# Kernel optimization log

Measured on AMD Instinct MI355X. Metric: run time of the kernel, lower is better.

## Reference

```python
import jax, jax.numpy as jnp
import numpy as np

B, T, C = 2, 2048, 2048
H, D = 16, 128


def _rope(x, cos, sin):
    # x: [B,H,T,D], cos/sin: [T,D//2]
    half = x.shape[-1] // 2
    x1, x2 = x[..., :half], x[..., half:]
    c = cos[None, None, :, :]
    s = sin[None, None, :, :]
    return jnp.concatenate([x1 * c - x2 * s, x1 * s + x2 * c], axis=-1)


def setup_inputs() -> dict:
    key = jax.random.key(0)
    k1, k2, k3, k4, k5 = jax.random.split(key, 5)
    x = jax.random.normal(k1, (B, T, C), dtype=jnp.float32)
    cos = jax.random.uniform(k2, (T, D // 2), dtype=jnp.float32)
    sin = jax.random.uniform(k3, (T, D // 2), dtype=jnp.float32)
    scale = 1.0 / np.sqrt(C)
    W_qkv = jax.random.normal(k4, (C, 3 * C), dtype=jnp.float32) * scale
    W_proj = jax.random.normal(k5, (C, C), dtype=jnp.float32) * scale
    return {"x": x, "cos": cos, "sin": sin, "W_qkv": W_qkv, "W_proj": W_proj}


def reference(x, cos, sin, W_qkv, W_proj):
    Bx, Tx, Cx = x.shape
    qkv = x @ W_qkv  # [B,T,3C]
    q, k, v = jnp.split(qkv, 3, axis=-1)
    # [B,T,C] -> [B,H,T,D]
    q = q.reshape(Bx, Tx, H, D).transpose(0, 2, 1, 3)
    k = k.reshape(Bx, Tx, H, D).transpose(0, 2, 1, 3)
    v = v.reshape(Bx, Tx, H, D).transpose(0, 2, 1, 3)
    q = _rope(q, cos, sin)
    k = _rope(k, cos, sin)
    # causal SDPA
    scores = jnp.einsum("bhqd,bhkd->bhqk", q, k) / jnp.sqrt(jnp.float32(D))
    causal = jnp.tril(jnp.ones((Tx, Tx), dtype=bool))
    scores = jnp.where(causal[None, None], scores, jnp.finfo(scores.dtype).min)
    attn = jax.nn.softmax(scores, axis=-1)
    out = jnp.einsum("bhqk,bhkd->bhqd", attn, v)
    out = out.transpose(0, 2, 1, 3).reshape(Bx, Tx, Cx)
    return out @ W_proj
```

## Files before the change

kernel.cpp:

```cpp
#include <hip/hip_runtime.h>
#include <stdint.h>

#define B_  2
#define T_  2048
#define C_  2048
#define H_  16
#define D_  128
#define BH_ 32
#define M_  4096

typedef __attribute__((ext_vector_type(8))) __bf16  bf16x8;
typedef __attribute__((ext_vector_type(4))) float   floatx4;
typedef __attribute__((ext_vector_type(4))) ushort  ushortx4;

__device__ __forceinline__ ushort f2bf(float f) {
    union { float f; uint32_t u; } v; v.f = f;
    return (ushort)((v.u + 0x7fffu + ((v.u >> 16) & 1u)) >> 16);
}

__device__ __forceinline__ float bf2f(ushort u) {
    union { uint32_t u; float f; } v; v.u = ((uint32_t)u) << 16;
    return v.f;
}

__device__ __forceinline__ floatx4 mfma_bf16(bf16x8 a, bf16x8 b, floatx4 c) {
    return __builtin_amdgcn_mfma_f32_16x16x32_bf16(a, b, c, 0, 0, 0);
}

__device__ __forceinline__ void async16(const ushort* g, ushort* l) {
    __builtin_amdgcn_global_load_lds(
        (const __attribute__((address_space(1))) uint32_t*)g,
        (__attribute__((address_space(3))) uint32_t*)l, 16, 0, 0);
}

__global__ __launch_bounds__(256) void convert_bf16(
    const float* __restrict__ X, ushort* __restrict__ Xb)
{
    const int i = blockIdx.x * 256 + threadIdx.x;
    const float4 v = ((const float4*)X)[i];
    ushortx4 p = { f2bf(v.x), f2bf(v.y), f2bf(v.z), f2bf(v.w) };
    ((ushortx4*)Xb)[i] = p;
}

__global__ __launch_bounds__(256) void transpose_w(
    const float* __restrict__ W, ushort* __restrict__ Wt, int Kdim, int Ndim)
{
    __shared__ float tile[32][33];
    const int n0 = blockIdx.x * 32, k0 = blockIdx.y * 32;
    const int tx = threadIdx.x, ty = threadIdx.y;
    #pragma unroll
    for (int j = 0; j < 4; j++)
        tile[ty + j*8][tx] = W[(size_t)(k0 + ty + j*8) * Ndim + n0 + tx];
    __syncthreads();
    #pragma unroll
    for (int j = 0; j < 4; j++)
        Wt[(size_t)(n0 + ty + j*8) * Kdim + k0 + tx] = f2bf(tile[tx][ty + j*8]);
}

#define BM 128
#define BN 128
#define BK 32

__global__ __launch_bounds__(256) void gemm_bt(
    const ushort* __restrict__ A, const ushort* __restrict__ Bt,
    float* __restrict__ Co, int Ndim, int Kdim)
{
    __shared__ __align__(16) ushort As[BM * BK];
    __shared__ __align__(16) ushort Bs[BN * BK];
    const int tid  = threadIdx.x;
    const int lane = tid & 63;
    const int w    = tid >> 6;
    const int wm   = (w >> 1) * 64;
    const int wn   = (w & 1) * 64;
    const int lr   = lane & 15;
    const int quad = lane >> 4;
    const int srow = lane >> 2;
    const int soff = (lane & 3) * 8;

    const ushort* Ablk = A  + (size_t)(blockIdx.y * BM) * Kdim;
    const ushort* Bblk = Bt + (size_t)(blockIdx.x * BN) * Kdim;

    floatx4 acc[4][4];
    #pragma unroll
    for (int i = 0; i < 4; i++)
        #pragma unroll
        for (int j = 0; j < 4; j++)
            acc[i][j] = (floatx4){0.f, 0.f, 0.f, 0.f};

    for (int k0 = 0; k0 < Kdim; k0 += BK) {
        __syncthreads();
        #pragma unroll
        for (int j = 0; j < 2; j++) {
            const int row = w * 32 + j * 16 + srow;
            async16(Ablk + (size_t)row * Kdim + k0 + soff,
                    As + (w * 32 + j * 16) * BK);
            async16(Bblk + (size_t)row * Kdim + k0 + soff,
                    Bs + (w * 32 + j * 16) * BK);
        }
        __syncthreads();

        bf16x8 af[4], bfr[4];
        #pragma unroll
        for (int mi = 0; mi < 4; mi++)
            af[mi] = *(const bf16x8*)(&As[(wm + mi*16 + lr) * BK + quad * 8]);
        #pragma unroll
        for (int ni = 0; ni < 4; ni++)
            bfr[ni] = *(const bf16x8*)(&Bs[(wn + ni*16 + lr) * BK + quad * 8]);
        #pragma unroll
        for (int mi = 0; mi < 4; mi++)
            #pragma unroll
            for (int ni = 0; ni < 4; ni++)
                acc[mi][ni] = mfma_bf16(af[mi], bfr[ni], acc[mi][ni]);
    }

    const size_t row0 = (size_t)blockIdx.y * BM + wm;
    const size_t col0 = (size_t)blockIdx.x * BN + wn;
    #pragma unroll
    for (int mi = 0; mi < 4; mi++)
        #pragma unroll
        for (int ni = 0; ni < 4; ni++)
            #pragma unroll
            for (int r = 0; r < 4; r++)
                Co[(row0 + mi*16 + quad*4 + r) * (size_t)Ndim + col0 + ni*16 + lr]
                    = acc[mi][ni][r];
}

__global__ __launch_bounds__(256) void gemm_qkv(
    const ushort* __restrict__ A, const ushort* __restrict__ Bt,
    const float* __restrict__ cosb, const float* __restrict__ sinb,
    ushort* __restrict__ qb, ushort* __restrict__ kbf, ushort* __restrict__ vt)
{
    __shared__ __align__(16) ushort smem[17408];
    ushort* As = smem;
    ushort* Bs = smem + 4096;

    const int tid  = threadIdx.x;
    const int lane = tid & 63;
    const int w    = tid >> 6;
    const int wm   = (w >> 1) * 64;
    const int wn   = (w & 1) * 64;
    const int lr   = lane & 15;
    const int quad = lane >> 4;
    const int srow = lane >> 2;
    const int soff = (lane & 3) * 8;

    const int Kdim = C_;
    const ushort* Ablk = A  + (size_t)(blockIdx.y * BM) * Kdim;
    const ushort* Bblk = Bt + (size_t)(blockIdx.x * BN) * Kdim;

    floatx4 acc[4][4];
    #pragma unroll
    for (int i = 0; i < 4; i++)
        #pragma unroll
        for (int j = 0; j < 4; j++)
            acc[i][j] = (floatx4){0.f, 0.f, 0.f, 0.f};

    for (int k0 = 0; k0 < Kdim; k0 += BK) {
        __syncthreads();
        #pragma unroll
        for (int j = 0; j < 2; j++) {
            const int row = w * 32 + j * 16 + srow;
            async16(Ablk + (size_t)row * Kdim + k0 + soff,
                    As + (w * 32 + j * 16) * BK);
            async16(Bblk + (size_t)row * Kdim + k0 + soff,
                    Bs + (w * 32 + j * 16) * BK);
        }
        __syncthreads();

        bf16x8 af[4], bfr[4];
        #pragma unroll
        for (int mi = 0; mi < 4; mi++)
            af[mi] = *(const bf16x8*)(&As[(wm + mi*16 + lr) * BK + quad * 8]);
        #pragma unroll
        for (int ni = 0; ni < 4; ni++)
            bfr[ni] = *(const bf16x8*)(&Bs[(wn + ni*16 + lr) * BK + quad * 8]);
        #pragma unroll
        for (int mi = 0; mi < 4; mi++)
            #pragma unroll
            for (int ni = 0; ni < 4; ni++)
                acc[mi][ni] = mfma_bf16(af[mi], bfr[ni], acc[mi][ni]);
    }

    const int h   = blockIdx.x & 15;
    const int qt  = blockIdx.x >> 4;
    const int b   = blockIdx.y >> 4;
    const int t0g = (blockIdx.y & 15) * 128;
    const int bh  = b * 16 + h;

    __syncthreads();

    if (qt < 2) {
        #pragma unroll
        for (int mi = 0; mi < 4; mi++)
            #pragma unroll
            for (int ni = 0; ni < 4; ni++)
                #pragma unroll
                for (int r = 0; r < 4; r++) {
                    const int t = wm + mi*16 + quad*4 + r;
                    const int d = wn + ni*16 + lr;
                    smem[t * 136 + d] = f2bf(acc[mi][ni][r]);
                }
        __syncthreads();

        const int t  = tid >> 1;
        const int c0 = (tid & 1) * 32;
        bf16x8 x1v[4], x2v[4];
        #pragma unroll
        for (int u = 0; u < 4; u++) {
            x1v[u] = *(const bf16x8*)(smem + t * 136 + c0 + u * 8);
            x2v[u] = *(const bf16x8*)(smem + t * 136 + 64 + c0 + u * 8);
        }
        const float4* cp4 = (const float4*)(cosb + (size_t)(t0g + t) * 64 + c0);
        const float4* sp4 = (const float4*)(sinb + (size_t)(t0g + t) * 64 + c0);
        ushort* outp = (qt == 0 ? qb : kbf) + ((size_t)bh * T_ + t0g + t) * D_;
        #pragma unroll
        for (int u = 0; u < 4; u++) {
            float cc[8], ss[8];
            *(float4*)(cc)     = cp4[u * 2];
            *(float4*)(cc + 4) = cp4[u * 2 + 1];
            *(float4*)(ss)     = sp4[u * 2];
            *(float4*)(ss + 4) = sp4[u * 2 + 1];
            ushortx4 lo0, lo1, hi0, hi1;
            #pragma unroll
            for (int e = 0; e < 8; e++) {
                const float x1 = (float)x1v[u][e];
                const float x2 = (float)x2v[u][e];
                const ushort vlo = f2bf(x1 * cc[e] - x2 * ss[e]);
                const ushort vhi = f2bf(x1 * ss[e] + x2 * cc[e]);
                if (e < 4) { lo0[e] = vlo; hi0[e] = vhi; }
                else       { lo1[e-4] = vlo; hi1[e-4] = vhi; }
            }
            *(ushortx4*)(outp + c0 + u*8)          = lo0;
            *(ushortx4*)(outp + c0 + u*8 + 4)      = lo1;
            *(ushortx4*)(outp + 64 + c0 + u*8)     = hi0;
            *(ushortx4*)(outp + 64 + c0 + u*8 + 4) = hi1;
        }
    } else {
        #pragma unroll
        for (int mi = 0; mi < 4; mi++)
            #pragma unroll
            for (int ni = 0; ni < 4; ni++)
                #pragma unroll
                for (int r = 0; r < 4; r++) {
                    const int t = wm + mi*16 + quad*4 + r;
                    const int d = wn + ni*16 + lr;
                    smem[d * 128 + (t & 7) + 8 * ((t >> 3) ^ (d & 15))]
                        = f2bf(acc[mi][ni][r]);
                }
        __syncthreads();

        const int d    = tid >> 1;
        const int half = tid & 1;
        ushort* outp = vt + ((size_t)bh * D_ + d) * T_ + t0g + half * 64;
        #pragma unroll
        for (int u = 0; u < 8; u++) {
            const int gu = half * 8 + u;
            bf16x8 vv = *(const bf16x8*)(smem + d * 128 + 8 * (gu ^ (d & 15)));
            *(bf16x8*)(outp + u * 8) = vv;
        }
    }
}

__global__ __launch_bounds__(256, 4) void flash_attn(
    const ushort* __restrict__ qb, const ushort* __restrict__ kb,
    const ushort* __restrict__ vt, ushort* __restrict__ attnoutb)
{
    __shared__ __align__(16) ushort kt_s[64 * 128];
    __shared__ __align__(16) ushort vt_s[128 * 64];
    __shared__ __align__(16) ushort pl_s[4][16 * 40];

    const int w    = threadIdx.x >> 6;
    const int lane = threadIdx.x & 63;
    const int lr   = lane & 15;
    const int quad = lane >> 4;

    const int bh = blockIdx.x & 31;
    const int m  = 31 - (blockIdx.x >> 5);
    const int qt = 4 * m + w;
    const int qbase = qt * 16;
    const int nk = m + 1;
    const int bb = bh >> 4, hh = bh & 15;

    const ushort* kbp = kb + (size_t)bh * T_ * D_;
    const ushort* vbp = vt + (size_t)bh * D_ * T_;
    ushort* pl = pl_s[w];

    bf16x8 qf[4];
    const ushort* qrow = qb + ((size_t)bh * T_ + qbase + lr) * D_ + quad * 8;
    #pragma unroll
    for (int kc = 0; kc < 4; kc++)
        qf[kc] = *(const bf16x8*)(qrow + kc * 32);

    floatx4 o[8];
    #pragma unroll
    for (int dc = 0; dc < 8; dc++) o[dc] = (floatx4){0.f, 0.f, 0.f, 0.f};
    floatx4 lac = (floatx4){0.f, 0.f, 0.f, 0.f};

    const __bf16 one = (__bf16)1.0f;
    const bf16x8 ones = {one, one, one, one, one, one, one, one};
    const float SCL  = 0.08838834764831845f * 1.4426950408889634f;
    const float BIAS = 23.083120654223414f;

    const int krow4 = lane >> 4;
    const int kunit = lane & 15;
    const int vrow8 = lane >> 3;
    const int vunit = lane & 7;

    for (int kt = 0; kt < nk; ++kt) {
        const int kb0 = kt * 64;
        __syncthreads();
        #pragma unroll
        for (int j = 0; j < 4; j++) {
            const int row = w * 16 + j * 4 + krow4;
            const ushort* gp = kbp + (size_t)(kb0 + row) * D_
                                   + ((kunit ^ (row & 15)) << 3);
            async16(gp, kt_s + (w * 16 + j * 4) * 128);
        }
        #pragma unroll
        for (int j = 0; j < 4; j++) {
            const int row = w * 32 + j * 8 + vrow8;
            const ushort* gp = vbp + (size_t)row * T_ + kb0
                                   + ((vunit ^ (row & 7)) << 3);
            async16(gp, vt_s + (w * 32 + j * 8) * 64);
        }
        __syncthreads();

        #pragma unroll
        for (int half = 0; half < 2; ++half) {
            floatx4 st[2];
            #pragma unroll
            for (int jj = 0; jj < 2; ++jj) {
                const int j = half * 2 + jj;
                floatx4 s = (floatx4){0.f, 0.f, 0.f, 0.f};
                const int kl = j * 16 + lr;
                #pragma unroll
                for (int kc = 0; kc < 4; kc++) {
                    bf16x8 af = *(const bf16x8*)(
                        kt_s + kl * 128 + ((((kc << 2) | quad) ^ lr) << 3));
                    s = mfma_bf16(af, qf[kc], s);
                }
                st[jj] = s;
            }
            #pragma unroll
            for (int jj = 0; jj < 2; ++jj) {
                const int j = half * 2 + jj;
                const int kg0 = kb0 + j * 16 + quad * 4;
                float p[4];
                #pragma unroll
                for (int r = 0; r < 4; r++) {
                    float e = __builtin_amdgcn_exp2f(fmaf(st[jj][r], SCL, -BIAS));
                    p[r] = (kg0 + r > qbase + lr) ? 0.f : e;
                }
                uint2 pk;
                pk.x = (uint32_t)f2bf(p[0]) | ((uint32_t)f2bf(p[1]) << 16);
                pk.y = (uint32_t)f2bf(p[2]) | ((uint32_t)f2bf(p[3]) << 16);
                *(uint2*)(pl + lr * 40 + jj * 16 + quad * 4) = pk;
            }
            bf16x8 pf = *(const bf16x8*)(pl + lr * 40 + quad * 8);
            lac = mfma_bf16(pf, ones, lac);
            #pragma unroll
            for (int dc = 0; dc < 8; dc++) {
                const int d = dc * 16 + lr;
                bf16x8 vf = *(const bf16x8*)(
                    vt_s + d * 64 + ((((half << 2) | quad) ^ (lr & 7)) << 3));
                o[dc] = mfma_bf16(pf, vf, o[dc]);
            }
        }
    }

    #pragma unroll
    for (int dc = 0; dc < 8; dc++)
        #pragma unroll
        for (int r = 0; r < 4; r++) {
            const int trow = qbase + quad * 4 + r;
            attnoutb[((size_t)(bb * T_ + trow)) * C_ + hh * D_ + dc * 16 + lr]
                = f2bf(o[dc][r] / lac[r]);
        }
}

extern "C" void kernel_launch(void* const* d_in, const int* in_sizes, int n_in,
                              void* d_out, int out_size, void* d_ws, size_t ws_size,
                              hipStream_t stream)
{
    (void)in_sizes; (void)n_in; (void)out_size; (void)ws_size;
    const float* x     = (const float*)d_in[0];
    const float* cosb  = (const float*)d_in[1];
    const float* sinb  = (const float*)d_in[2];
    const float* Wqkv  = (const float*)d_in[3];
    const float* Wproj = (const float*)d_in[4];
    float* out = (float*)d_out;

    char* ws = (char*)d_ws;
    ushort* xb       = (ushort*)(ws);
    ushort* Wtq      = (ushort*)(ws + 16777216);
    ushort* Wtp      = (ushort*)(ws + 41943040);
    ushort* qb       = (ushort*)(ws + 50331648);
    ushort* kbf      = (ushort*)(ws + 67108864);
    ushort* vt       = (ushort*)(ws + 83886080);
    ushort* attnoutb = (ushort*)(ws + 100663296);

    dim3 tb32(32, 8);
    transpose_w<<<dim3(3 * C_ / 32, C_ / 32), tb32, 0, stream>>>(Wqkv, Wtq, C_, 3 * C_);
    transpose_w<<<dim3(C_ / 32, C_ / 32),     tb32, 0, stream>>>(Wproj, Wtp, C_, C_);
    convert_bf16<<<(M_ * C_ / 4) / 256, 256, 0, stream>>>(x, xb);

    gemm_qkv<<<dim3(3 * C_ / BN, M_ / BM), 256, 0, stream>>>(
        xb, Wtq, cosb, sinb, qb, kbf, vt);

    flash_attn<<<BH_ * 32, 256, 0, stream>>>(qb, kbf, vt, attnoutb);

    gemm_bt<<<dim3(C_ / BN, M_ / BM), 256, 0, stream>>>(attnoutb, Wtp, out, C_, C_);
}
```

Measured before the change: 410.4 us.

## Replace GEMMs with 256x256 tiled, double-buffered 8-phase pipelined MFMA kernels

Both the QKV and output projection GEMMs move from 128x128x32 single-buffered tiles to 256x256x64 tiles run by 512-thread blocks. The new K-loop double-buffers LDS with async global-to-LDS loads and interleaves them with four MFMA phases per step, using barriers and setprio to hide memory latency. It also adds XOR-swizzled LDS layouts to avoid bank conflicts and an XCD-aware block-index remap. The QKV epilogue is reworked for the larger tile so each tile covers two heads, with wider 16-byte stores. The cost is more LDS and register pressure and a fragile hand-tuned barrier and waitcnt schedule; the projection GEMM launches only 128 blocks.

```diff
diff --git a/kernel.cpp b/kernel.cpp
--- a/kernel.cpp
+++ b/kernel.cpp
@@ -12,6 +12,7 @@
 typedef __attribute__((ext_vector_type(8))) __bf16  bf16x8;
 typedef __attribute__((ext_vector_type(4))) float   floatx4;
 typedef __attribute__((ext_vector_type(4))) ushort  ushortx4;
+typedef __attribute__((ext_vector_type(8))) ushort  ushortx8;
 
 __device__ __forceinline__ ushort f2bf(float f) {
     union { float f; uint32_t u; } v; v.f = f;
@@ -57,205 +58,294 @@
         Wt[(size_t)(n0 + ty + j*8) * Kdim + k0 + tx] = f2bf(tile[tx][ty + j*8]);
 }
 
-#define BM 128
-#define BN 128
-#define BK 32
-
-__global__ __launch_bounds__(256) void gemm_bt(
+struct FragA { bf16x8 f[4][2]; };
+struct FragB { bf16x8 f[2][2]; };
+
+__device__ __forceinline__ void load_a(FragA& fa, const ushort* Ab, int base,
+                                       int lr, int quad)
+{
+    #pragma unroll
+    for (int mi2 = 0; mi2 < 4; mi2++)
+        #pragma unroll
+        for (int kk = 0; kk < 2; kk++) {
+            const int row = base + mi2 * 16 + lr;
+            fa.f[mi2][kk] = *(const bf16x8*)(
+                Ab + row * 64 + (((kk * 4 + quad) ^ (lr & 7)) << 3));
+        }
+}
+
+__device__ __forceinline__ void load_b(FragB& fb, const ushort* Bb, int base,
+                                       int lr, int quad)
+{
+    #pragma unroll
+    for (int ni2 = 0; ni2 < 2; ni2++)
+        #pragma unroll
+        for (int kk = 0; kk < 2; kk++) {
+            const int row = base + ni2 * 16 + lr;
+            fb.f[ni2][kk] = *(const bf16x8*)(
+                Bb + row * 64 + (((kk * 4 + quad) ^ (lr & 7)) << 3));
+        }
+}
+
+__device__ __forceinline__ void mfma_quad(floatx4 (&acc)[8][4], const FragA& fa,
+                                          const FragB& fb, int mh, int nh)
+{
+    #pragma unroll
+    for (int mi2 = 0; mi2 < 4; mi2++)
+        #pragma unroll
+        for (int ni2 = 0; ni2 < 2; ni2++)
+            #pragma unroll
+            for (int kk = 0; kk < 2; kk++)
+                acc[mh*4 + mi2][nh*2 + ni2] =
+                    mfma_bf16(fa.f[mi2][kk], fb.f[ni2][kk],
+                              acc[mh*4 + mi2][nh*2 + ni2]);
+}
+
+__device__ __forceinline__ void stage64(const ushort* __restrict__ gsrc,
+                                        ushort* ldst, int blk, int k0, int tid)
+{
+    const int lane = tid & 63;
+    const int w8   = tid >> 6;
+    const int rl   = lane >> 3;
+    const int u    = lane & 7;
+    const int row  = (blk << 6) + (w8 << 3) + rl;
+    const ushort* g = gsrc + (size_t)row * C_ + k0 + ((u ^ rl) << 3);
+    async16(g, ldst + (blk << 12) + (w8 << 9));
+}
+
+__device__ __forceinline__ void kloop_8ph(
+    const ushort* __restrict__ Ablk, const ushort* __restrict__ Bblk,
+    ushort* lds, floatx4 (&acc)[8][4], int tid)
+{
+    const int lane = tid & 63;
+    const int w    = tid >> 6;
+    const int wr   = w >> 2;
+    const int wc   = w & 3;
+    const int lr   = lane & 15;
+    const int quad = lane >> 4;
+
+    #pragma unroll
+    for (int blk = 0; blk < 4; blk++) {
+        stage64(Ablk, lds,         blk, 0, tid);
+        stage64(Bblk, lds + 32768, blk, 0, tid);
+    }
+    #pragma unroll
+    for (int blk = 0; blk < 4; blk++) {
+        stage64(Ablk, lds + 16384, blk, 64, tid);
+        stage64(Bblk, lds + 49152, blk, 64, tid);
+    }
+    asm volatile("s_waitcnt vmcnt(8)" ::: "memory");
+    __builtin_amdgcn_sched_barrier(0);
+    __builtin_amdgcn_s_barrier();
+
+    FragA fa0, fa1;
+    FragB fb0, fb1;
+
+    #pragma unroll 2
+    for (int t = 0; t < 32; ++t) {
+        const int p = t & 1;
+        ushort* Ab = lds + (p << 14);
+        ushort* Bb = lds + 32768 + (p << 14);
+        const int k2 = (t + 2) << 6;
+        const bool st = (t < 30);
+
+        load_a(fa0, Ab, wr * 128, lr, quad);
+        load_b(fb0, Bb, wc * 64, lr, quad);
+        __builtin_amdgcn_s_barrier();
+        asm volatile("s_waitcnt lgkmcnt(0)" ::: "memory");
+        __builtin_amdgcn_sched_barrier(0);
+        __builtin_amdgcn_s_setprio(1);
+        mfma_quad(acc, fa0, fb0, 0, 0);
+        __builtin_amdgcn_s_setprio(0);
+        __builtin_amdgcn_s_barrier();
+
+        load_b(fb1, Bb, wc * 64 + 32, lr, quad);
+        if (st) { stage64(Ablk, Ab, 0, k2, tid);
+                  stage64(Ablk, Ab, 2, k2, tid); }
+        __builtin_amdgcn_s_barrier();
+        asm volatile("s_waitcnt lgkmcnt(0)" ::: "memory");
+        __builtin_amdgcn_sched_barrier(0);
+        __builtin_amdgcn_s_setprio(1);
+        mfma_quad(acc, fa0, fb1, 0, 1);
+        __builtin_amdgcn_s_setprio(0);
+        __builtin_amdgcn_s_barrier();
+
+        load_a(fa1, Ab, wr * 128 + 64, lr, quad);
+        if (st) { stage64(Bblk, Bb, 0, k2, tid);
+                  stage64(Bblk, Bb, 1, k2, tid);
+                  stage64(Bblk, Bb, 2, k2, tid); }
+        __builtin_amdgcn_s_barrier();
+        asm volatile("s_waitcnt lgkmcnt(0)" ::: "memory");
+        __builtin_amdgcn_sched_barrier(0);
+        __builtin_amdgcn_s_setprio(1);
+        mfma_quad(acc, fa1, fb0, 1, 0);
+        __builtin_amdgcn_s_setprio(0);
+        __builtin_amdgcn_s_barrier();
+
+        if (st) { stage64(Bblk, Bb, 3, k2, tid);
+                  stage64(Ablk, Ab, 1, k2, tid);
+                  stage64(Ablk, Ab, 3, k2, tid); }
+        if (st) asm volatile("s_waitcnt vmcnt(8)" ::: "memory");
+        else    asm volatile("s_waitcnt vmcnt(0)" ::: "memory");
+        __builtin_amdgcn_sched_barrier(0);
+        __builtin_amdgcn_s_barrier();
+        __builtin_amdgcn_s_setprio(1);
+        mfma_quad(acc, fa1, fb1, 1, 1);
+        __builtin_amdgcn_s_setprio(0);
+        __builtin_amdgcn_s_barrier();
+    }
+}
+
+__global__ __launch_bounds__(512, 2) void gemm_bt_8ph(
     const ushort* __restrict__ A, const ushort* __restrict__ Bt,
-    float* __restrict__ Co, int Ndim, int Kdim)
-{
-    __shared__ __align__(16) ushort As[BM * BK];
-    __shared__ __align__(16) ushort Bs[BN * BK];
+    float* __restrict__ Co)
+{
+    __shared__ __align__(16) ushort lds[65536];
+
     const int tid  = threadIdx.x;
     const int lane = tid & 63;
     const int w    = tid >> 6;
-    const int wm   = (w >> 1) * 64;
-    const int wn   = (w & 1) * 64;
+    const int wr   = w >> 2;
+    const int wc   = w & 3;
     const int lr   = lane & 15;
     const int quad = lane >> 4;
-    const int srow = lane >> 2;
-    const int soff = (lane & 3) * 8;
-
-    const ushort* Ablk = A  + (size_t)(blockIdx.y * BM) * Kdim;
-    const ushort* Bblk = Bt + (size_t)(blockIdx.x * BN) * Kdim;
-
-    floatx4 acc[4][4];
-    #pragma unroll
-    for (int i = 0; i < 4; i++)
+
+    int bid = (int)blockIdx.x;
+    bid = (bid & 7) * 16 + (bid >> 3);
+    const int bx = bid & 7;
+    const int by = bid >> 3;
+
+    const ushort* Ablk = A  + (size_t)(by * 256) * C_;
+    const ushort* Bblk = Bt + (size_t)(bx * 256) * C_;
+
+    floatx4 acc[8][4];
+    #pragma unroll
+    for (int i = 0; i < 8; i++)
         #pragma unroll
         for (int j = 0; j < 4; j++)
             acc[i][j] = (floatx4){0.f, 0.f, 0.f, 0.f};
 
-    for (int k0 = 0; k0 < Kdim; k0 += BK) {
-        __syncthreads();
-        #pragma unroll
-        for (int j = 0; j < 2; j++) {
-            const int row = w * 32 + j * 16 + srow;
-            async16(Ablk + (size_t)row * Kdim + k0 + soff,
-                    As + (w * 32 + j * 16) * BK);
-            async16(Bblk + (size_t)row * Kdim + k0 + soff,
-                    Bs + (w * 32 + j * 16) * BK);
-        }
-        __syncthreads();
-
-        bf16x8 af[4], bfr[4];
-        #pragma unroll
-        for (int mi = 0; mi < 4; mi++)
-            af[mi] = *(const bf16x8*)(&As[(wm + mi*16 + lr) * BK + quad * 8]);
+    kloop_8ph(Ablk, Bblk, lds, acc, tid);
+
+    const size_t row0 = (size_t)by * 256 + wr * 128;
+    const size_t col0 = (size_t)bx * 256 + wc * 64;
+    #pragma unroll
+    for (int mi = 0; mi < 8; mi++)
         #pragma unroll
         for (int ni = 0; ni < 4; ni++)
-            bfr[ni] = *(const bf16x8*)(&Bs[(wn + ni*16 + lr) * BK + quad * 8]);
-        #pragma unroll
-        for (int mi = 0; mi < 4; mi++)
-            #pragma unroll
-            for (int ni = 0; ni < 4; ni++)
-                acc[mi][ni] = mfma_bf16(af[mi], bfr[ni], acc[mi][ni]);
-    }
-
-    const size_t row0 = (size_t)blockIdx.y * BM + wm;
-    const size_t col0 = (size_t)blockIdx.x * BN + wn;
-    #pragma unroll
-    for (int mi = 0; mi < 4; mi++)
-        #pragma unroll
-        for (int ni = 0; ni < 4; ni++)
             #pragma unroll
             for (int r = 0; r < 4; r++)
-                Co[(row0 + mi*16 + quad*4 + r) * (size_t)Ndim + col0 + ni*16 + lr]
+                Co[(row0 + mi*16 + quad*4 + r) * (size_t)C_ + col0 + ni*16 + lr]
                     = acc[mi][ni][r];
 }
 
-__global__ __launch_bounds__(256) void gemm_qkv(
+__global__ __launch_bounds__(512, 2) void gemm_qkv_8ph(
     const ushort* __restrict__ A, const ushort* __restrict__ Bt,
     const float* __restrict__ cosb, const float* __restrict__ sinb,
     ushort* __restrict__ qb, ushort* __restrict__ kbf, ushort* __restrict__ vt)
 {
-    __shared__ __align__(16) ushort smem[17408];
-    ushort* As = smem;
-    ushort* Bs = smem + 4096;
+    __shared__ __align__(16) ushort lds[65536];
 
     const int tid  = threadIdx.x;
     const int lane = tid & 63;
     const int w    = tid >> 6;
-    const int wm   = (w >> 1) * 64;
-    const int wn   = (w & 1) * 64;
+    const int wr   = w >> 2;
+    const int wc   = w & 3;
     const int lr   = lane & 15;
     const int quad = lane >> 4;
-    const int srow = lane >> 2;
-    const int soff = (lane & 3) * 8;
-
-    const int Kdim = C_;
-    const ushort* Ablk = A  + (size_t)(blockIdx.y * BM) * Kdim;
-    const ushort* Bblk = Bt + (size_t)(blockIdx.x * BN) * Kdim;
-
-    floatx4 acc[4][4];
-    #pragma unroll
-    for (int i = 0; i < 4; i++)
+
+    int bid = (int)blockIdx.x;
+    bid = (bid & 7) * 48 + (bid >> 3);
+    const int bx = bid % 24;
+    const int by = bid / 24;
+
+    const ushort* Ablk = A  + (size_t)(by * 256) * C_;
+    const ushort* Bblk = Bt + (size_t)(bx * 256) * C_;
+
+    floatx4 acc[8][4];
+    #pragma unroll
+    for (int i = 0; i < 8; i++)
         #pragma unroll
         for (int j = 0; j < 4; j++)
             acc[i][j] = (floatx4){0.f, 0.f, 0.f, 0.f};
 
-    for (int k0 = 0; k0 < Kdim; k0 += BK) {
-        __syncthreads();
-        #pragma unroll
-        for (int j = 0; j < 2; j++) {
-            const int row = w * 32 + j * 16 + srow;
-            async16(Ablk + (size_t)row * Kdim + k0 + soff,
-                    As + (w * 32 + j * 16) * BK);
-            async16(Bblk + (size_t)row * Kdim + k0 + soff,
-                    Bs + (w * 32 + j * 16) * BK);
-        }
-        __syncthreads();
-
-        bf16x8 af[4], bfr[4];
-        #pragma unroll
-        for (int mi = 0; mi < 4; mi++)
-            af[mi] = *(const bf16x8*)(&As[(wm + mi*16 + lr) * BK + quad * 8]);
-        #pragma unroll
-        for (int ni = 0; ni < 4; ni++)
-            bfr[ni] = *(const bf16x8*)(&Bs[(wn + ni*16 + lr) * BK + quad * 8]);
-        #pragma unroll
-        for (int mi = 0; mi < 4; mi++)
-            #pragma unroll
-            for (int ni = 0; ni < 4; ni++)
-                acc[mi][ni] = mfma_bf16(af[mi], bfr[ni], acc[mi][ni]);
-    }
-
-    const int h   = blockIdx.x & 15;
-    const int qt  = blockIdx.x >> 4;
-    const int b   = blockIdx.y >> 4;
-    const int t0g = (blockIdx.y & 15) * 128;
-    const int bh  = b * 16 + h;
+    kloop_8ph(Ablk, Bblk, lds, acc, tid);
+
+    const int qt  = bx >> 3;
+    const int h0  = (bx & 7) << 1;
+    const int b   = by >> 3;
+    const int t0g = (by & 7) << 8;
 
     __syncthreads();
 
     if (qt < 2) {
         #pragma unroll
-        for (int mi = 0; mi < 4; mi++)
+        for (int mi = 0; mi < 8; mi++)
             #pragma unroll
             for (int ni = 0; ni < 4; ni++)
                 #pragma unroll
                 for (int r = 0; r < 4; r++) {
-                    const int t = wm + mi*16 + quad*4 + r;
-                    const int d = wn + ni*16 + lr;
-                    smem[t * 136 + d] = f2bf(acc[mi][ni][r]);
+                    const int tt = wr * 128 + mi * 16 + quad * 4 + r;
+                    const int cc = wc * 64 + ni * 16 + lr;
+                    lds[tt * 256 + ((((cc >> 3) ^ (tt & 31)) << 3) | (cc & 7))]
+                        = f2bf(acc[mi][ni][r]);
                 }
         __syncthreads();
 
-        const int t  = tid >> 1;
-        const int c0 = (tid & 1) * 32;
-        bf16x8 x1v[4], x2v[4];
-        #pragma unroll
-        for (int u = 0; u < 4; u++) {
-            x1v[u] = *(const bf16x8*)(smem + t * 136 + c0 + u * 8);
-            x2v[u] = *(const bf16x8*)(smem + t * 136 + 64 + c0 + u * 8);
-        }
-        const float4* cp4 = (const float4*)(cosb + (size_t)(t0g + t) * 64 + c0);
-        const float4* sp4 = (const float4*)(sinb + (size_t)(t0g + t) * 64 + c0);
-        ushort* outp = (qt == 0 ? qb : kbf) + ((size_t)bh * T_ + t0g + t) * D_;
-        #pragma unroll
-        for (int u = 0; u < 4; u++) {
+        const int trow = tid >> 1;
+        const int hsel = tid & 1;
+        const int tg   = t0g + trow;
+        const int bh   = b * 16 + h0 + hsel;
+        ushort* outp = (qt == 0 ? qb : kbf) + ((size_t)bh * T_ + tg) * D_;
+        const float4* cp4 = (const float4*)(cosb + (size_t)tg * 64);
+        const float4* sp4 = (const float4*)(sinb + (size_t)tg * 64);
+        const ushort* rowp = lds + trow * 256;
+        const int tw = trow & 31;
+        #pragma unroll
+        for (int u = 0; u < 8; u++) {
+            bf16x8 x1 = *(const bf16x8*)(rowp + (((hsel * 16 + u)     ^ tw) << 3));
+            bf16x8 x2 = *(const bf16x8*)(rowp + (((hsel * 16 + 8 + u) ^ tw) << 3));
             float cc[8], ss[8];
             *(float4*)(cc)     = cp4[u * 2];
             *(float4*)(cc + 4) = cp4[u * 2 + 1];
             *(float4*)(ss)     = sp4[u * 2];
             *(float4*)(ss + 4) = sp4[u * 2 + 1];
-            ushortx4 lo0, lo1, hi0, hi1;
+            ushortx8 lo, hi;
             #pragma unroll
             for (int e = 0; e < 8; e++) {
-                const float x1 = (float)x1v[u][e];
-                const float x2 = (float)x2v[u][e];
-                const ushort vlo = f2bf(x1 * cc[e] - x2 * ss[e]);
-                const ushort vhi = f2bf(x1 * ss[e] + x2 * cc[e]);
-                if (e < 4) { lo0[e] = vlo; hi0[e] = vhi; }
-                else       { lo1[e-4] = vlo; hi1[e-4] = vhi; }
+                const float x1f = (float)x1[e];
+                const float x2f = (float)x2[e];
+                lo[e] = f2bf(x1f * cc[e] - x2f * ss[e]);
+                hi[e] = f2bf(x1f * ss[e] + x2f * cc[e]);
             }
-            *(ushortx4*)(outp + c0 + u*8)          = lo0;
-            *(ushortx4*)(outp + c0 + u*8 + 4)      = lo1;
-            *(ushortx4*)(outp + 64 + c0 + u*8)     = hi0;
-            *(ushortx4*)(outp + 64 + c0 + u*8 + 4) = hi1;
+            *(ushortx8*)(outp + u * 8)      = lo;
+            *(ushortx8*)(outp + 64 + u * 8) = hi;
         }
     } else {
         #pragma unroll
-        for (int mi = 0; mi < 4; mi++)
+        for (int mi = 0; mi < 8; mi++)
             #pragma unroll
             for (int ni = 0; ni < 4; ni++)
                 #pragma unroll
                 for (int r = 0; r < 4; r++) {
-                    const int t = wm + mi*16 + quad*4 + r;
-                    const int d = wn + ni*16 + lr;
-                    smem[d * 128 + (t & 7) + 8 * ((t >> 3) ^ (d & 15))]
+                    const int tt = wr * 128 + mi * 16 + quad * 4 + r;
+                    const int cc = wc * 64 + ni * 16 + lr;
+                    lds[cc * 256 + ((((tt >> 3) ^ (cc & 31)) << 3) | (tt & 7))]
                         = f2bf(acc[mi][ni][r]);
                 }
         __syncthreads();
 
-        const int d    = tid >> 1;
-        const int half = tid & 1;
-        ushort* outp = vt + ((size_t)bh * D_ + d) * T_ + t0g + half * 64;
-        #pragma unroll
-        for (int u = 0; u < 8; u++) {
-            const int gu = half * 8 + u;
-            bf16x8 vv = *(const bf16x8*)(smem + d * 128 + 8 * (gu ^ (d & 15)));
+        const int c  = tid >> 1;
+        const int hT = tid & 1;
+        const int hh = c >> 7;
+        const int d  = c & 127;
+        const int bh = b * 16 + h0 + hh;
+        const ushort* rowp = lds + c * 256;
+        const int cw = c & 31;
+        ushort* outp = vt + ((size_t)bh * D_ + d) * T_ + t0g + hT * 128;
+        #pragma unroll
+        for (int u = 0; u < 16; u++) {
+            bf16x8 vv = *(const bf16x8*)(rowp + (((hT * 16 + u) ^ cw) << 3));
             *(bf16x8*)(outp + u * 8) = vv;
         }
     }
@@ -404,10 +494,9 @@
     transpose_w<<<dim3(C_ / 32, C_ / 32),     tb32, 0, stream>>>(Wproj, Wtp, C_, C_);
     convert_bf16<<<(M_ * C_ / 4) / 256, 256, 0, stream>>>(x, xb);
 
-    gemm_qkv<<<dim3(3 * C_ / BN, M_ / BM), 256, 0, stream>>>(
-        xb, Wtq, cosb, sinb, qb, kbf, vt);
+    gemm_qkv_8ph<<<384, 512, 0, stream>>>(xb, Wtq, cosb, sinb, qb, kbf, vt);
 
     flash_attn<<<BH_ * 32, 256, 0, stream>>>(qb, kbf, vt, attnoutb);
 
-    gemm_bt<<<dim3(C_ / BN, M_ / BM), 256, 0, stream>>>(attnoutb, Wtp, out, C_, C_);
-}
+    gemm_bt_8ph<<<128, 512, 0, stream>>>(attnoutb, Wtp, out);
+}
```

Measured after the change: 412.7 us. About the same (+0.6%).

## Double-buffer K/V tiles in flash attention to overlap loads with compute

Applied to the files above, without the earlier changes.

Makes the K and V shared-memory tiles double-buffered: the next tile's async loads are issued before the current tile is computed, and one barrier per iteration replaces two. The goal is to hide global-to-LDS latency behind the MFMA work. This doubles LDS use to about 69 KB per block and lowers the launch-bounds occupancy hint from 4 to 2 blocks. Correctness relies on the async loads having finished by the barrier at the end of each iteration.

```diff
diff --git a/kernel.cpp b/kernel.cpp
--- a/kernel.cpp
+++ b/kernel.cpp
@@ -261,12 +261,12 @@
     }
 }
 
-__global__ __launch_bounds__(256, 4) void flash_attn(
+__global__ __launch_bounds__(256, 2) void flash_attn(
     const ushort* __restrict__ qb, const ushort* __restrict__ kb,
     const ushort* __restrict__ vt, ushort* __restrict__ attnoutb)
 {
-    __shared__ __align__(16) ushort kt_s[64 * 128];
-    __shared__ __align__(16) ushort vt_s[128 * 64];
+    __shared__ __align__(16) ushort kt_s[2][64 * 128];
+    __shared__ __align__(16) ushort vt_s[2][128 * 64];
     __shared__ __align__(16) ushort pl_s[4][16 * 40];
 
     const int w    = threadIdx.x >> 6;
@@ -285,6 +285,11 @@
     const ushort* vbp = vt + (size_t)bh * D_ * T_;
     ushort* pl = pl_s[w];
 
+    const int krow4 = lane >> 4;
+    const int kunit = lane & 15;
+    const int vrow8 = lane >> 3;
+    const int vunit = lane & 7;
+
     bf16x8 qf[4];
     const ushort* qrow = qb + ((size_t)bh * T_ + qbase + lr) * D_ + quad * 8;
     #pragma unroll
@@ -301,29 +306,49 @@
     const float SCL  = 0.08838834764831845f * 1.4426950408889634f;
     const float BIAS = 23.083120654223414f;
 
-    const int krow4 = lane >> 4;
-    const int kunit = lane & 15;
-    const int vrow8 = lane >> 3;
-    const int vunit = lane & 7;
-
-    for (int kt = 0; kt < nk; ++kt) {
-        const int kb0 = kt * 64;
-        __syncthreads();
+    {
+        const int kb0 = 0;
         #pragma unroll
         for (int j = 0; j < 4; j++) {
             const int row = w * 16 + j * 4 + krow4;
             const ushort* gp = kbp + (size_t)(kb0 + row) * D_
                                    + ((kunit ^ (row & 15)) << 3);
-            async16(gp, kt_s + (w * 16 + j * 4) * 128);
+            async16(gp, kt_s[0] + (w * 16 + j * 4) * 128);
         }
         #pragma unroll
         for (int j = 0; j < 4; j++) {
             const int row = w * 32 + j * 8 + vrow8;
             const ushort* gp = vbp + (size_t)row * T_ + kb0
                                    + ((vunit ^ (row & 7)) << 3);
-            async16(gp, vt_s + (w * 32 + j * 8) * 64);
-        }
-        __syncthreads();
+            async16(gp, vt_s[0] + (w * 32 + j * 8) * 64);
+        }
+    }
+    __syncthreads();
+
+    for (int kt = 0; kt < nk; ++kt) {
+        const int bsel = kt & 1;
+        const int kb0  = kt * 64;
+
+        if (kt + 1 < nk) {
+            const int kb1 = kb0 + 64;
+            #pragma unroll
+            for (int j = 0; j < 4; j++) {
+                const int row = w * 16 + j * 4 + krow4;
+                const ushort* gp = kbp + (size_t)(kb1 + row) * D_
+                                       + ((kunit ^ (row & 15)) << 3);
+                async16(gp, kt_s[bsel ^ 1] + (w * 16 + j * 4) * 128);
+            }
+            #pragma unroll
+            for (int j = 0; j < 4; j++) {
+                const int row = w * 32 + j * 8 + vrow8;
+                const ushort* gp = vbp + (size_t)row * T_ + kb1
+                                       + ((vunit ^ (row & 7)) << 3);
+                async16(gp, vt_s[bsel ^ 1] + (w * 32 + j * 8) * 64);
+            }
+        }
+
+        const ushort* kbuf = kt_s[bsel];
+        const ushort* vbuf = vt_s[bsel];
 
         #pragma unroll
         for (int half = 0; half < 2; ++half) {
@@ -336,7 +361,7 @@
                 #pragma unroll
                 for (int kc = 0; kc < 4; kc++) {
                     bf16x8 af = *(const bf16x8*)(
-                        kt_s + kl * 128 + ((((kc << 2) | quad) ^ lr) << 3));
+                        kbuf + kl * 128 + ((((kc << 2) | quad) ^ lr) << 3));
                     s = mfma_bf16(af, qf[kc], s);
                 }
                 st[jj] = s;
@@ -362,10 +387,12 @@
             for (int dc = 0; dc < 8; dc++) {
                 const int d = dc * 16 + lr;
                 bf16x8 vf = *(const bf16x8*)(
-                    vt_s + d * 64 + ((((half << 2) | quad) ^ (lr & 7)) << 3));
+                    vbuf + d * 64 + ((((half << 2) | quad) ^ (lr & 7)) << 3));
                 o[dc] = mfma_bf16(pf, vf, o[dc]);
             }
         }
+
+        __syncthreads();
     }
 
     #pragma unroll
```

After: 406.4 us. Within noise of the previous version (-1.0%).
